# Optimization experiments

Hardware: AMD Instinct MI355X
Metric: run time of the kernel (lower is better)

The kernel has to match this reference:

```python
import jax, jax.numpy as jnp
import numpy as np

HASH_CODE_LEN = 8  # config['hash_code_len']
EPS = 1e-12

def _l2norm(x):
    n = jnp.sqrt(jnp.sum(x * x, axis=-1, keepdims=True))
    return x / jnp.maximum(n, EPS)

def setup_inputs() -> dict:
    key = jax.random.key(0)
    k1, k2, k3, k4 = jax.random.split(key, 4)
    B, H, S, D = 2, 12, 2048, 64
    Q = jax.random.normal(k1, (B, H, S, D), dtype=jnp.float32)
    K = jax.random.normal(k2, (B, H, S, D), dtype=jnp.float32)
    V = jax.random.normal(k3, (B, H, S, D), dtype=jnp.float32)
    mask = jnp.ones((B, S), dtype=jnp.float32)
    conv_w = jax.random.normal(k4, (H, 1, 3, 1), dtype=jnp.float32)  # depthwise Conv2d weight [H,1,w,1]
    return {"Q": Q, "K": K, "V": V, "mask": mask, "conv_w": conv_w}

def reference(Q, K, V, mask, conv_w):
    B, H, S, D = Q.shape
    # conv branch: depthwise conv over the sequence axis, per head (groups=num_head)
    Vm = V * mask[:, None, :, None]  # [B,H,S,D]
    conv_V = jax.lax.conv_general_dilated(
        Vm, conv_w,
        window_strides=(1, 1),
        padding=[(1, 1), (0, 0)],  # (conv_window//2, 0)
        dimension_numbers=("NCHW", "OIHW", "NCHW"),
        feature_group_count=H,
    )
    # YOSO attention: exact expectation of LSH cumulation.
    # collision prob of unit vectors q,k over hash_code_len bits: (1 - acos(q.k)/pi)^tau
    qn = _l2norm(Q)
    kn = _l2norm(K)
    dots = jnp.einsum("bhsd,bhtd->bhst", qn, kn)
    dots = jnp.clip(dots, -1.0, 1.0)
    W = (1.0 - jnp.arccos(dots) / jnp.pi) ** HASH_CODE_LEN  # [B,H,S,S]
    W = W * mask[:, None, None, :]  # key mask
    X = jnp.einsum("bhst,bhtd->bhsd", W, V)
    X = X * mask[:, None, :, None]  # query mask
    X = _l2norm(X)  # kernel.normalize(X)
    return X + conv_V
```

## Files before the change

### kernel.cpp

```cpp
#include <hip/hip_runtime.h>
#include <hip/hip_bf16.h>
#include <math.h>

#define NB 2
#define NH 12
#define NS 2048
#define ND 64
#define NBH (NB * NH)
#define TILE_USHORT 4096
#define QK_TILE_BLOCKS 1536
#define V_BLOCKS (NBH * 32)

typedef __attribute__((ext_vector_type(8))) short short8;
typedef __attribute__((ext_vector_type(4))) float floatx4;
typedef __attribute__((ext_vector_type(2))) float float2v;

__device__ __forceinline__ unsigned short f32_to_bf16_rne(float f) {
  unsigned int u = __float_as_uint(f);
  u += 0x7fffu + ((u >> 16) & 1u);
  return (unsigned short)(u >> 16);
}

__device__ __forceinline__ unsigned int bf16rne_bits(float f) {
  unsigned int u = __float_as_uint(f);
  return u + 0x7fffu + ((u >> 16) & 1u);
}

__device__ __forceinline__ unsigned int pack2_bf16_rne(float lo, float hi) {
  return __builtin_amdgcn_perm(bf16rne_bits(hi), bf16rne_bits(lo), 0x07060302);
}

__device__ __forceinline__ unsigned int pack_bf16_trunc(float lo, float hi) {
  return __builtin_amdgcn_perm(__float_as_uint(hi), __float_as_uint(lo), 0x07060302);
}

__device__ __forceinline__ float2v mk2(float x) { return (float2v){x, x}; }
__device__ __forceinline__ float2v max2(float2v a, float2v b) {
  return (float2v){fmaxf(a[0], b[0]), fmaxf(a[1], b[1])};
}
__device__ __forceinline__ float2v abs2(float2v a) {
  return (float2v){fabsf(a[0]), fabsf(a[1])};
}

__device__ __forceinline__ float yoso_f_exact(float d) {
  const float c0 = 0.49996030f;
  const float c1 = -0.06751822f;
  const float c2 = 0.02363774f;
  const float c3 = -0.00596174f;
  float a = fminf(fabsf(d), 1.0f);
  float p = fmaf(fmaf(fmaf(c3, a, c2), a, c1), a, c0);
  float u = sqrtf(1.0f - a) * p;
  return (d >= 0.0f) ? (1.0f - u) : u;
}

__device__ __forceinline__ void gload_lds16(const unsigned short* src,
                                            unsigned short* lds_dst) {
  __builtin_amdgcn_global_load_lds(
      (const __attribute__((address_space(1))) unsigned int*)(const void*)src,
      (__attribute__((address_space(3))) unsigned int*)(void*)lds_dst,
      16, 0, 0);
}

__global__ __launch_bounds__(256) void prep_all(
    const float* __restrict__ Q, const float* __restrict__ K,
    const float* __restrict__ V, const float* __restrict__ mask,
    unsigned short* __restrict__ qimg, unsigned short* __restrict__ kimg,
    unsigned short* __restrict__ vimg) {
  int blk = blockIdx.x;
  if (blk < QK_TILE_BLOCKS) {
    const float* src = Q;
    unsigned short* dst = qimg;
    if (blk >= 768) { src = K; dst = kimg; blk -= 768; }
    int ti  = blk;
    int tid = threadIdx.x;
    int w   = tid >> 6;
    int l   = tid & 63;
    int nl  = l & 15;
    int dq  = l >> 4;

    const float* row = src + ((size_t)ti * 64 + w * 16 + nl) * ND + dq * 8;
    float4 a0 = *(const float4*)(row);
    float4 a1 = *(const float4*)(row + 4);
    float4 b0 = *(const float4*)(row + 32);
    float4 b1 = *(const float4*)(row + 36);

    float ss = a0.x*a0.x + a0.y*a0.y + a0.z*a0.z + a0.w*a0.w
             + a1.x*a1.x + a1.y*a1.y + a1.z*a1.z + a1.w*a1.w
             + b0.x*b0.x + b0.y*b0.y + b0.z*b0.z + b0.w*b0.w
             + b1.x*b1.x + b1.y*b1.y + b1.z*b1.z + b1.w*b1.w;
    ss += __shfl_xor(ss, 16, 64);
    ss += __shfl_xor(ss, 32, 64);
    float rn = 1.0f / fmaxf(sqrtf(ss), 1e-12f);

    uint4 o0, o1;
    o0.x = pack2_bf16_rne(a0.x * rn, a0.y * rn);
    o0.y = pack2_bf16_rne(a0.z * rn, a0.w * rn);
    o0.z = pack2_bf16_rne(a1.x * rn, a1.y * rn);
    o0.w = pack2_bf16_rne(a1.z * rn, a1.w * rn);
    o1.x = pack2_bf16_rne(b0.x * rn, b0.y * rn);
    o1.y = pack2_bf16_rne(b0.z * rn, b0.w * rn);
    o1.z = pack2_bf16_rne(b1.x * rn, b1.y * rn);
    o1.w = pack2_bf16_rne(b1.z * rn, b1.w * rn);

    unsigned short* op = dst + (size_t)ti * TILE_USHORT + w * 512 + l * 8;
    *(uint4*)(op)            = o0;
    *(uint4*)(op + 4 * 512)  = o1;
  } else {
    int vb = blk - QK_TILE_BLOCKS;
    int bh = vb >> 5, kt = vb & 31, t0 = kt * 64;
    int b  = bh / NH;
    __shared__ float sT[64][65];
    int tid = threadIdx.x;
    int tr = tid >> 2;
    int dc = (tid & 3) * 16;
    float m = mask[b * NS + t0 + tr];
    const float* vp = V + ((size_t)bh * NS + t0 + tr) * ND + dc;
    #pragma unroll
    for (int jj = 0; jj < 16; jj += 4) {
      float4 v = *(const float4*)(vp + jj);
      sT[dc + jj + 0][tr] = v.x * m;
      sT[dc + jj + 1][tr] = v.y * m;
      sT[dc + jj + 2][tr] = v.z * m;
      sT[dc + jj + 3][tr] = v.w * m;
    }
    __syncthreads();
    int dr = tid >> 2;
    unsigned short* op = vimg + (size_t)(bh * 32 + kt) * TILE_USHORT;
    #pragma unroll
    for (int g = 0; g < 2; ++g) {
      int combo = (tid & 3) * 2 + g;
      int kk2 = combo >> 2;
      int qd  = combo & 3;
      uint4 u;
      int tb = kk2 * 32 + qd * 4;
      u.x = (unsigned int)f32_to_bf16_rne(sT[dr][tb + 0]) |
            ((unsigned int)f32_to_bf16_rne(sT[dr][tb + 1]) << 16);
      u.y = (unsigned int)f32_to_bf16_rne(sT[dr][tb + 2]) |
            ((unsigned int)f32_to_bf16_rne(sT[dr][tb + 3]) << 16);
      u.z = (unsigned int)f32_to_bf16_rne(sT[dr][tb + 16]) |
            ((unsigned int)f32_to_bf16_rne(sT[dr][tb + 17]) << 16);
      u.w = (unsigned int)f32_to_bf16_rne(sT[dr][tb + 18]) |
            ((unsigned int)f32_to_bf16_rne(sT[dr][tb + 19]) << 16);
      int frag = kk2 * 4 + (dr >> 4);
      int ln   = qd * 16 + (dr & 15);
      *(uint4*)(op + frag * 512 + ln * 8) = u;
    }
  }
}

__global__ __launch_bounds__(256, 3) void yoso_main(
    const unsigned short* __restrict__ qimg, const unsigned short* __restrict__ kimg,
    const unsigned short* __restrict__ vimg, const float* __restrict__ V,
    const float* __restrict__ mask, const float* __restrict__ conv_w,
    float* __restrict__ out) {
  int bid = blockIdx.x;
  int lid = (bid & 7) * 96 + (bid >> 3);
  int bh = lid >> 5;
  int b  = bh / NH;
  int h  = bh % NH;
  int qt = lid & 31;
  int s0 = qt * 64;

  __shared__ unsigned short kbuf[4][4096];

  int tid  = threadIdx.x;
  int wv   = tid >> 6;
  int lane = tid & 63;
  int lq   = lane & 15;
  int quad = lane >> 4;
  int qs   = wv & 1;
  int kp   = wv >> 1;

  uint4 qfrag[2][2];
  {
    const unsigned short* qtile = qimg + (size_t)(bh * 32 + qt) * TILE_USHORT;
    #pragma unroll
    for (int j = 0; j < 2; ++j)
      #pragma unroll
      for (int kk = 0; kk < 2; ++kk)
        qfrag[j][kk] = *(const uint4*)(qtile + (kk * 4 + qs * 2 + j) * 512 + lane * 8);
  }

  float w0 = conv_w[h * 3 + 0], w1 = conv_w[h * 3 + 1], w2 = conv_w[h * 3 + 2];

  floatx4 acc[2][4];
  #pragma unroll
  for (int j = 0; j < 2; ++j)
    #pragma unroll
    for (int fd = 0; fd < 4; ++fd) acc[j][fd] = (floatx4){0.f, 0.f, 0.f, 0.f};

  const unsigned short* kb  = kimg + (size_t)bh * 32 * TILE_USHORT;
  const unsigned short* vbI = vimg + (size_t)bh * 32 * TILE_USHORT;

  const float P0 = 0.3183098862f;
  const float P1 = 0.0530516477f;
  const float P2 = 0.0238732415f;
  const float P3 = 0.0142098402f;
  const float P4 = 0.0096701727f;
  const float P5 = 0.0071212906f;

  auto stage_pair = [&](int pb, int t0) {
    #pragma unroll
    for (int c = 0; c < 4; ++c) {
      int region = wv * 4 + c;
      int tsel   = region >> 3;
      int piece  = region & 7;
      gload_lds16(kb + (size_t)(t0 + tsel) * TILE_USHORT + piece * 512 + lane * 8,
                  &kbuf[pb + tsel][piece * 512]);
    }
  };

  stage_pair(0, 0);
  __syncthreads();

  #pragma unroll 1
  for (int r = 0; r < 16; ++r) {
    int pb = (r & 1) * 2;
    if (r < 15) stage_pair(2 - pb, 2 * r + 2);

    int kt = 2 * r + kp;
    const unsigned short* sb = kbuf[pb + kp];

    uint4 kf[2][4];
    #pragma unroll
    for (int kk = 0; kk < 2; ++kk)
      #pragma unroll
      for (int ft = 0; ft < 4; ++ft)
        kf[kk][ft] = *(const uint4*)(sb + (kk * 4 + ft) * 512 + lane * 8);

    floatx4 sc[2][4];
    #pragma unroll
    for (int j = 0; j < 2; ++j)
      #pragma unroll
      for (int ft = 0; ft < 4; ++ft) sc[j][ft] = (floatx4){0.f, 0.f, 0.f, 0.f};
    #pragma unroll
    for (int kk = 0; kk < 2; ++kk) {
      #pragma unroll
      for (int j = 0; j < 2; ++j) {
        short8 bq = *(const short8*)&qfrag[j][kk];
        #pragma unroll
        for (int ft = 0; ft < 4; ++ft)
          sc[j][ft] = __builtin_amdgcn_mfma_f32_16x16x32_bf16(
              *(const short8*)&kf[kk][ft], bq, sc[j][ft], 0, 0, 0);
      }
    }

    const unsigned short* vtile = vbI + (size_t)kt * TILE_USHORT;
    uint4 vf[2][4];
    #pragma unroll
    for (int kk2 = 0; kk2 < 2; ++kk2)
      #pragma unroll
      for (int fd = 0; fd < 4; ++fd)
        vf[kk2][fd] = *(const uint4*)(vtile + (kk2 * 4 + fd) * 512 + lane * 8);

    {
      float2v mxy = mk2(0.f);
      #pragma unroll
      for (int j = 0; j < 2; ++j)
        #pragma unroll
        for (int ft = 0; ft < 4; ++ft) {
          float2v* p = (float2v*)&sc[j][ft];
          mxy = max2(mxy, max2(abs2(p[0]), abs2(p[1])));
        }
      float mx = fmaxf(mxy[0], mxy[1]);
      if (__builtin_expect(__any(mx > 0.82f), 0)) {
        #pragma unroll
        for (int j = 0; j < 2; ++j)
          #pragma unroll
          for (int ft = 0; ft < 4; ++ft)
            #pragma unroll
            for (int r2 = 0; r2 < 4; ++r2) {
              float f = yoso_f_exact(sc[j][ft][r2]);
              float f2 = f * f;
              float f4 = f2 * f2;
              sc[j][ft][r2] = f4 * f4;
            }
      } else {
        float2v c5 = mk2(P5), c4 = mk2(P4), c3 = mk2(P3), c2 = mk2(P2),
                c1 = mk2(P1), c0 = mk2(P0), hf = mk2(0.5f);
        #pragma unroll
        for (int j = 0; j < 2; ++j)
          #pragma unroll
          for (int ft = 0; ft < 4; ++ft) {
            float2v* p = (float2v*)&sc[j][ft];
            #pragma unroll
            for (int hh = 0; hh < 2; ++hh) {
              float2v d = p[hh];
              float2v y = d * d;
              float2v pp = ((((c5 * y + c4) * y + c3) * y + c2) * y + c1) * y + c0;
              float2v f = pp * d + hf;
              float2v f2 = f * f;
              float2v f4 = f2 * f2;
              p[hh] = f4 * f4;
            }
          }
      }
    }

    #pragma unroll
    for (int j = 0; j < 2; ++j) {
      #pragma unroll
      for (int kk2 = 0; kk2 < 2; ++kk2) {
        uint4 u;
        u.x = pack_bf16_trunc(sc[j][2 * kk2][0], sc[j][2 * kk2][1]);
        u.y = pack_bf16_trunc(sc[j][2 * kk2][2], sc[j][2 * kk2][3]);
        u.z = pack_bf16_trunc(sc[j][2 * kk2 + 1][0], sc[j][2 * kk2 + 1][1]);
        u.w = pack_bf16_trunc(sc[j][2 * kk2 + 1][2], sc[j][2 * kk2 + 1][3]);
        short8 bw = *(short8*)&u;
        #pragma unroll
        for (int fd = 0; fd < 4; ++fd)
          acc[j][fd] = __builtin_amdgcn_mfma_f32_16x16x32_bf16(
              *(const short8*)&vf[kk2][fd], bw, acc[j][fd], 0, 0, 0);
      }
    }

    __syncthreads();
  }

  float* xch = (float*)&kbuf[0][0];
  if (kp == 1) {
    #pragma unroll
    for (int j = 0; j < 2; ++j) {
      float* wr = xch + (qs * 2 + j) * 1088;
      #pragma unroll
      for (int fd = 0; fd < 4; ++fd)
        #pragma unroll
        for (int r2 = 0; r2 < 4; ++r2)
          wr[lq * 68 + fd * 16 + quad * 4 + r2] = acc[j][fd][r2];
    }
  }
  __syncthreads();
  if (kp == 0) {
    #pragma unroll
    for (int j = 0; j < 2; ++j) {
      const float* rd = xch + (qs * 2 + j) * 1088;
      #pragma unroll
      for (int fd = 0; fd < 4; ++fd)
        #pragma unroll
        for (int r2 = 0; r2 < 4; ++r2)
          acc[j][fd][r2] += rd[lq * 68 + fd * 16 + quad * 4 + r2];
    }

    #pragma unroll
    for (int j = 0; j < 2; ++j) {
      int s = s0 + qs * 32 + j * 16 + lq;
      float qm  = mask[b * NS + s];
      float qm0 = (s > 0) ? mask[b * NS + s - 1] : 0.f;
      float qm2 = (s < NS - 1) ? mask[b * NS + s + 1] : 0.f;
      float ssum = 0.f;
      #pragma unroll
      for (int fd = 0; fd < 4; ++fd)
        #pragma unroll
        for (int r2 = 0; r2 < 4; ++r2) {
          float x = acc[j][fd][r2] * qm;
          acc[j][fd][r2] = x;
          ssum += x * x;
        }
      ssum += __shfl_xor(ssum, 16, 64);
      ssum += __shfl_xor(ssum, 32, 64);
      float rn = 1.0f / fmaxf(sqrtf(ssum), 1e-12f);

      const float* vfull = V + ((size_t)bh * NS + s) * ND;
      #pragma unroll
      for (int fd = 0; fd < 4; ++fd) {
        int d = fd * 16 + quad * 4;
        float4 vc1 = *(const float4*)(vfull + d);
        float4 cv;
        cv.x = w1 * vc1.x * qm; cv.y = w1 * vc1.y * qm;
        cv.z = w1 * vc1.z * qm; cv.w = w1 * vc1.w * qm;
        if (s > 0) {
          float4 vc0 = *(const float4*)(vfull - ND + d);
          cv.x += w0 * vc0.x * qm0; cv.y += w0 * vc0.y * qm0;
          cv.z += w0 * vc0.z * qm0; cv.w += w0 * vc0.w * qm0;
        }
        if (s < NS - 1) {
          float4 vc2 = *(const float4*)(vfull + ND + d);
          cv.x += w2 * vc2.x * qm2; cv.y += w2 * vc2.y * qm2;
          cv.z += w2 * vc2.z * qm2; cv.w += w2 * vc2.w * qm2;
        }
        float4 o;
        o.x = acc[j][fd][0] * rn + cv.x;
        o.y = acc[j][fd][1] * rn + cv.y;
        o.z = acc[j][fd][2] * rn + cv.z;
        o.w = acc[j][fd][3] * rn + cv.w;
        *(float4*)(out + ((size_t)bh * NS + s) * ND + d) = o;
      }
    }
  }
}

extern "C" void kernel_launch(void* const* d_in, const int* in_sizes, int n_in,
                              void* d_out, int out_size, void* d_ws, size_t ws_size,
                              hipStream_t stream) {
  const float* Q      = (const float*)d_in[0];
  const float* K      = (const float*)d_in[1];
  const float* V      = (const float*)d_in[2];
  const float* mask   = (const float*)d_in[3];
  const float* conv_w = (const float*)d_in[4];
  float* out = (float*)d_out;

  const size_t seg = (size_t)NBH * NS * ND * sizeof(unsigned short);
  unsigned short* qimg = (unsigned short*)d_ws;
  unsigned short* kimg = (unsigned short*)((char*)d_ws + seg);
  unsigned short* vimg = (unsigned short*)((char*)d_ws + 2 * seg);

  prep_all<<<QK_TILE_BLOCKS + V_BLOCKS, 256, 0, stream>>>(Q, K, V, mask, qimg, kimg, vimg);
  yoso_main<<<NBH * 32, 256, 0, stream>>>(qimg, kimg, vimg, V, mask, conv_w, out);
}
```

Before: 139.7 us.

## Split each key tile across two waves with 512-thread blocks and two-stage reduction

```diff
diff --git a/kernel.cpp b/kernel.cpp
--- a/kernel.cpp
+++ b/kernel.cpp
@@ -148,7 +148,7 @@
   }
 }
 
-__global__ __launch_bounds__(256, 3) void yoso_main(
+__global__ __launch_bounds__(512, 6) void yoso_main(
     const unsigned short* __restrict__ qimg, const unsigned short* __restrict__ kimg,
     const unsigned short* __restrict__ vimg, const float* __restrict__ V,
     const float* __restrict__ mask, const float* __restrict__ conv_w,
@@ -169,7 +169,8 @@
   int lq   = lane & 15;
   int quad = lane >> 4;
   int qs   = wv & 1;
-  int kp   = wv >> 1;
+  int kp   = (wv >> 1) & 1;
+  int tk   = wv >> 2;
 
   uint4 qfrag[2][2];
   {
@@ -201,8 +202,8 @@
 
   auto stage_pair = [&](int pb, int t0) {
     #pragma unroll
-    for (int c = 0; c < 4; ++c) {
-      int region = wv * 4 + c;
+    for (int c = 0; c < 2; ++c) {
+      int region = wv * 2 + c;
       int tsel   = region >> 3;
       int piece  = region & 7;
       gload_lds16(kb + (size_t)(t0 + tsel) * TILE_USHORT + piece * 512 + lane * 8,
@@ -221,45 +222,43 @@
     int kt = 2 * r + kp;
     const unsigned short* sb = kbuf[pb + kp];
 
-    uint4 kf[2][4];
+    uint4 kf[2][2];
     #pragma unroll
     for (int kk = 0; kk < 2; ++kk)
       #pragma unroll
-      for (int ft = 0; ft < 4; ++ft)
-        kf[kk][ft] = *(const uint4*)(sb + (kk * 4 + ft) * 512 + lane * 8);
-
-    floatx4 sc[2][4];
+      for (int fl = 0; fl < 2; ++fl)
+        kf[kk][fl] = *(const uint4*)(sb + (kk * 4 + tk * 2 + fl) * 512 + lane * 8);
+
+    floatx4 sc[2][2];
     #pragma unroll
     for (int j = 0; j < 2; ++j)
       #pragma unroll
-      for (int ft = 0; ft < 4; ++ft) sc[j][ft] = (floatx4){0.f, 0.f, 0.f, 0.f};
+      for (int fl = 0; fl < 2; ++fl) sc[j][fl] = (floatx4){0.f, 0.f, 0.f, 0.f};
     #pragma unroll
     for (int kk = 0; kk < 2; ++kk) {
       #pragma unroll
       for (int j = 0; j < 2; ++j) {
         short8 bq = *(const short8*)&qfrag[j][kk];
         #pragma unroll
-        for (int ft = 0; ft < 4; ++ft)
-          sc[j][ft] = __builtin_amdgcn_mfma_f32_16x16x32_bf16(
-              *(const short8*)&kf[kk][ft], bq, sc[j][ft], 0, 0, 0);
+        for (int fl = 0; fl < 2; ++fl)
+          sc[j][fl] = __builtin_amdgcn_mfma_f32_16x16x32_bf16(
+              *(const short8*)&kf[kk][fl], bq, sc[j][fl], 0, 0, 0);
       }
     }
 
     const unsigned short* vtile = vbI + (size_t)kt * TILE_USHORT;
-    uint4 vf[2][4];
-    #pragma unroll
-    for (int kk2 = 0; kk2 < 2; ++kk2)
-      #pragma unroll
-      for (int fd = 0; fd < 4; ++fd)
-        vf[kk2][fd] = *(const uint4*)(vtile + (kk2 * 4 + fd) * 512 + lane * 8);
+    uint4 vf[4];
+    #pragma unroll
+    for (int fd = 0; fd < 4; ++fd)
+      vf[fd] = *(const uint4*)(vtile + (tk * 4 + fd) * 512 + lane * 8);
 
     {
       float2v mxy = mk2(0.f);
       #pragma unroll
       for (int j = 0; j < 2; ++j)
         #pragma unroll
-        for (int ft = 0; ft < 4; ++ft) {
-          float2v* p = (float2v*)&sc[j][ft];
+        for (int fl = 0; fl < 2; ++fl) {
+          float2v* p = (float2v*)&sc[j][fl];
           mxy = max2(mxy, max2(abs2(p[0]), abs2(p[1])));
         }
       float mx = fmaxf(mxy[0], mxy[1]);
@@ -267,13 +266,13 @@
         #pragma unroll
         for (int j = 0; j < 2; ++j)
           #pragma unroll
-          for (int ft = 0; ft < 4; ++ft)
+          for (int fl = 0; fl < 2; ++fl)
             #pragma unroll
             for (int r2 = 0; r2 < 4; ++r2) {
-              float f = yoso_f_exact(sc[j][ft][r2]);
+              float f = yoso_f_exact(sc[j][fl][r2]);
               float f2 = f * f;
               float f4 = f2 * f2;
-              sc[j][ft][r2] = f4 * f4;
+              sc[j][fl][r2] = f4 * f4;
             }
       } else {
         float2v c5 = mk2(P5), c4 = mk2(P4), c3 = mk2(P3), c2 = mk2(P2),
@@ -281,8 +280,8 @@
         #pragma unroll
         for (int j = 0; j < 2; ++j)
           #pragma unroll
-          for (int ft = 0; ft < 4; ++ft) {
-            float2v* p = (float2v*)&sc[j][ft];
+          for (int fl = 0; fl < 2; ++fl) {
+            float2v* p = (float2v*)&sc[j][fl];
             #pragma unroll
             for (int hh = 0; hh < 2; ++hh) {
               float2v d = p[hh];
@@ -299,46 +298,67 @@
 
     #pragma unroll
     for (int j = 0; j < 2; ++j) {
-      #pragma unroll
-      for (int kk2 = 0; kk2 < 2; ++kk2) {
-        uint4 u;
-        u.x = pack_bf16_trunc(sc[j][2 * kk2][0], sc[j][2 * kk2][1]);
-        u.y = pack_bf16_trunc(sc[j][2 * kk2][2], sc[j][2 * kk2][3]);
-        u.z = pack_bf16_trunc(sc[j][2 * kk2 + 1][0], sc[j][2 * kk2 + 1][1]);
-        u.w = pack_bf16_trunc(sc[j][2 * kk2 + 1][2], sc[j][2 * kk2 + 1][3]);
-        short8 bw = *(short8*)&u;
-        #pragma unroll
-        for (int fd = 0; fd < 4; ++fd)
-          acc[j][fd] = __builtin_amdgcn_mfma_f32_16x16x32_bf16(
-              *(const short8*)&vf[kk2][fd], bw, acc[j][fd], 0, 0, 0);
-      }
+      uint4 u;
+      u.x = pack_bf16_trunc(sc[j][0][0], sc[j][0][1]);
+      u.y = pack_bf16_trunc(sc[j][0][2], sc[j][0][3]);
+      u.z = pack_bf16_trunc(sc[j][1][0], sc[j][1][1]);
+      u.w = pack_bf16_trunc(sc[j][1][2], sc[j][1][3]);
+      short8 bw = *(short8*)&u;
+      #pragma unroll
+      for (int fd = 0; fd < 4; ++fd)
+        acc[j][fd] = __builtin_amdgcn_mfma_f32_16x16x32_bf16(
+            *(const short8*)&vf[fd], bw, acc[j][fd], 0, 0, 0);
     }
 
     __syncthreads();
   }
 
   float* xch = (float*)&kbuf[0][0];
-  if (kp == 1) {
-    #pragma unroll
-    for (int j = 0; j < 2; ++j) {
-      float* wr = xch + (qs * 2 + j) * 1088;
+  if (tk == 1) {
+    #pragma unroll
+    for (int j = 0; j < 2; ++j) {
+      float* wr = xch + (((qs * 2 + kp) * 2 + j) << 10);
       #pragma unroll
       for (int fd = 0; fd < 4; ++fd)
         #pragma unroll
         for (int r2 = 0; r2 < 4; ++r2)
-          wr[lq * 68 + fd * 16 + quad * 4 + r2] = acc[j][fd][r2];
+          wr[(fd * 16 + quad * 4 + r2) * 16 + lq] = acc[j][fd][r2];
     }
   }
   __syncthreads();
-  if (kp == 0) {
-    #pragma unroll
-    for (int j = 0; j < 2; ++j) {
-      const float* rd = xch + (qs * 2 + j) * 1088;
+  if (tk == 0) {
+    #pragma unroll
+    for (int j = 0; j < 2; ++j) {
+      const float* rd = xch + (((qs * 2 + kp) * 2 + j) << 10);
       #pragma unroll
       for (int fd = 0; fd < 4; ++fd)
         #pragma unroll
         for (int r2 = 0; r2 < 4; ++r2)
-          acc[j][fd][r2] += rd[lq * 68 + fd * 16 + quad * 4 + r2];
+          acc[j][fd][r2] += rd[(fd * 16 + quad * 4 + r2) * 16 + lq];
+    }
+  }
+  __syncthreads();
+  if (tk == 0 && kp == 1) {
+    #pragma unroll
+    for (int j = 0; j < 2; ++j) {
+      float* wr = xch + (((qs * 2) + j) << 10);
+      #pragma unroll
+      for (int fd = 0; fd < 4; ++fd)
+        #pragma unroll
+        for (int r2 = 0; r2 < 4; ++r2)
+          wr[(fd * 16 + quad * 4 + r2) * 16 + lq] = acc[j][fd][r2];
+    }
+  }
+  __syncthreads();
+  if (tk == 0 && kp == 0) {
+    #pragma unroll
+    for (int j = 0; j < 2; ++j) {
+      const float* rd = xch + (((qs * 2) + j) << 10);
+      #pragma unroll
+      for (int fd = 0; fd < 4; ++fd)
+        #pragma unroll
+        for (int r2 = 0; r2 < 4; ++r2)
+          acc[j][fd][r2] += rd[(fd * 16 + quad * 4 + r2) * 16 + lq];
     }
 
     #pragma unroll
@@ -405,5 +425,5 @@
   unsigned short* vimg = (unsigned short*)((char*)d_ws + 2 * seg);
 
   prep_all<<<QK_TILE_BLOCKS + V_BLOCKS, 256, 0, stream>>>(Q, K, V, mask, qimg, kimg, vimg);
-  yoso_main<<<NBH * 32, 256, 0, stream>>>(qimg, kimg, vimg, V, mask, conv_w, out);
-}
+  yoso_main<<<NBH * 32, 512, 0, stream>>>(qimg, kimg, vimg, V, mask, conv_w, out);
+}
```

Measured after the change: 280.1 us. +100.5%, slower.
